# Optimization experiments

Measured on AMD Instinct MI355X. Metric: run time of the kernel, lower is better.

The kernel has to match this reference:

```python
import jax, jax.numpy as jnp
import numpy as np

B, C, N, F_IN = 8, 5, 512, 768
H, D_HID, D_OUT = 4, 128, 64
NEG_SLOPE = 0.2


def _gat_layer(h, mask, W, a_l, a_r, b, apply_relu):
    # h: [B,N,Fin], mask: [B,N,N] bool (mask[b,i,j]=True means edge i->j)
    Bn, Nn, _ = h.shape
    Hh, Dd = a_l.shape
    feat = (h @ W).reshape(Bn, Nn, Hh, Dd)              # [B,N,H,D]
    el = jnp.einsum('bnhd,hd->bnh', feat, a_l)          # src scores
    er = jnp.einsum('bnhd,hd->bnh', feat, a_r)          # dst scores
    e = jax.nn.leaky_relu(el[:, :, None, :] + er[:, None, :, :], NEG_SLOPE)  # [B,src,dst,H]
    m = mask[..., None]
    e = jnp.where(m, e, jnp.finfo(e.dtype).min)
    emax = jnp.max(e, axis=1, keepdims=True)
    p = jnp.where(m, jnp.exp(e - emax), 0.0)
    s = jnp.sum(p, axis=1, keepdims=True)
    alpha = p / jnp.maximum(s, 1e-9)                    # edge softmax over incoming edges per dst
    out = jnp.einsum('bijh,bihd->bjhd', alpha, feat)    # aggregate src features to dst
    out = out + b.reshape(1, 1, Hh, Dd)
    if apply_relu:
        out = jax.nn.relu(out)
    return out                                           # [B,N,H,D]


def setup_inputs() -> dict:
    key = jax.random.key(0)
    ks = jax.random.split(key, 16)
    x = jax.random.normal(ks[0], (B, C, N, F_IN), dtype=jnp.float32)
    adj = (jax.random.uniform(ks[1], (B, C, N, N)) < 0.1).astype(jnp.float32)
    node_nums = jnp.full((B,), N, dtype=jnp.int32)
    s = 0.02
    W0 = jax.random.normal(ks[2], (C, F_IN, H * D_HID)) * s
    al0 = jax.random.normal(ks[3], (C, H, D_HID)) * s
    ar0 = jax.random.normal(ks[4], (C, H, D_HID)) * s
    b0 = jnp.zeros((C, H * D_HID), jnp.float32)
    W1 = jax.random.normal(ks[5], (C, H * D_HID, H * D_HID)) * s
    al1 = jax.random.normal(ks[6], (C, H, D_HID)) * s
    ar1 = jax.random.normal(ks[7], (C, H, D_HID)) * s
    b1 = jnp.zeros((C, H * D_HID), jnp.float32)
    W2 = jax.random.normal(ks[8], (C, H * D_HID, H * D_OUT)) * s
    al2 = jax.random.normal(ks[9], (C, H, D_OUT)) * s
    ar2 = jax.random.normal(ks[10], (C, H, D_OUT)) * s
    b2 = jnp.zeros((C, H * D_OUT), jnp.float32)
    return dict(x=x, adj=adj, W0=W0, al0=al0, ar0=ar0, b0=b0,
                W1=W1, al1=al1, ar1=ar1, b1=b1,
                W2=W2, al2=al2, ar2=ar2, b2=b2, node_nums=node_nums)


def reference(x, adj, W0, al0, ar0, b0, W1, al1, ar1, b1, W2, al2, ar2, b2, node_nums):
    # Original concatenates per-batch node slices and takes channel 0 features only.
    h0 = x[:, 0]                       # [B,N,F_IN]
    logits_all = []
    for c in range(C):
        mask = adj[:, c] > 0           # [B,N,N]
        h = _gat_layer(h0, mask, W0[c], al0[c], ar0[c], b0[c].reshape(H, D_HID), True).reshape(B, N, H * D_HID)
        h = _gat_layer(h, mask, W1[c], al1[c], ar1[c], b1[c].reshape(H, D_HID), True).reshape(B, N, H * D_HID)
        out = _gat_layer(h, mask, W2[c], al2[c], ar2[c], b2[c].reshape(H, D_OUT), False).mean(axis=2)  # [B,N,D_OUT]
        logits_all.append(out)
    return jnp.concatenate(logits_all, axis=-1)  # [B,N,C*D_OUT]
```

## Files before the change

kernel.cpp:

```cpp
#include <hip/hip_runtime.h>

typedef unsigned int uint;
typedef unsigned short ushort_t;
typedef __attribute__((ext_vector_type(8))) short short8;
typedef __attribute__((ext_vector_type(4))) float f32x4;

#define NB 8
#define NC 5
#define NN 512
#define FIN 768
#define NH 4
#define MT 4096
#define LOG2E 1.4426950408889634f

#if __has_builtin(__builtin_amdgcn_exp2f)
#define EXP2F(v) __builtin_amdgcn_exp2f(v)
#else
#define EXP2F(v) __expf((v)*0.6931471805599453f)
#endif

__device__ __forceinline__ float b2f(ushort_t u){ uint x = ((uint)u)<<16; return __builtin_bit_cast(float, x); }
__device__ __forceinline__ ushort_t f2b(float f){
  uint u = __builtin_bit_cast(uint, f);
  u += 0x7FFFu + ((u>>16)&1u);
  return (ushort_t)(u>>16);
}
__device__ __forceinline__ ushort_t f2b_fast(float f){
  uint u = __builtin_bit_cast(uint, f);
  return (ushort_t)((u + 0x8000u)>>16);
}

#define GLL16(gp, lp) __builtin_amdgcn_global_load_lds( \
    (const __attribute__((address_space(1))) void*)(gp), \
    (__attribute__((address_space(3))) void*)(lp), 16, 0, 0)

__global__ __launch_bounds__(256) void prep(const float* __restrict__ x, ushort_t* __restrict__ h0b,
                                            const float* __restrict__ W0, ushort_t* __restrict__ Wt0,
                                            const float* __restrict__ W1, ushort_t* __restrict__ Wt1,
                                            const float* __restrict__ W2, ushort_t* __restrict__ Wt2,
                                            const float* __restrict__ adj, uint* __restrict__ adjB){
  __shared__ float tile[32][33];
  int bid = blockIdx.x, t = threadIdx.x;
  if (bid < 3072){
    int tid = bid*256 + t;
    int row = tid/192, q = tid%192;
    int b = row >> 9, n = row & 511;
    float4 v = *(const float4*)(x + ((size_t)(b*NC)*NN + n)*FIN + q*4);
    ushort4 o; o.x = f2b(v.x); o.y = f2b(v.y); o.z = f2b(v.z); o.w = f2b(v.w);
    *(ushort4*)(h0b + (size_t)row*FIN + q*4) = o;
  } else if (bid < 6912){
    const float* W; ushort_t* Wt; int K, N, c, x0, y0;
    if (bid < 4992){ int l = bid-3072; K=768; N=512; W=W0; Wt=Wt0; c=l/384; int r=l%384; x0=r%16; y0=r/16; }
    else if (bid < 6272){ int l = bid-4992; K=512; N=512; W=W1; Wt=Wt1; c=l/256; int r=l%256; x0=r%16; y0=r/16; }
    else { int l = bid-6272; K=512; N=256; W=W2; Wt=Wt2; c=l/128; int r=l%128; x0=r%8; y0=r/8; }
    int n0 = x0*32, k0 = y0*32;
    int tx = t & 31, ty = t >> 5;
    const float* Wp = W + (size_t)c*K*N;
    ushort_t* Wtp = Wt + (size_t)c*K*N;
    #pragma unroll
    for (int r=0;r<4;r++) tile[ty+r*8][tx] = Wp[(size_t)(k0+ty+r*8)*N + n0+tx];
    __syncthreads();
    #pragma unroll
    for (int r=0;r<4;r++) Wtp[(size_t)(n0+ty+r*8)*K + k0+tx] = f2b(tile[tx][ty+r*8]);
  } else {
    int l = bid - 6912;
    int iw = l & 15, zz = l >> 4;
    const float* ap = adj + (size_t)zz*NN*NN + (size_t)iw*32*NN;
    uint w0 = 0, w1 = 0;
    #pragma unroll 8
    for (int q=0;q<32;q++){
      if (ap[(size_t)q*NN + t]       > 0.f) w0 |= (1u<<q);
      if (ap[(size_t)q*NN + t + 256] > 0.f) w1 |= (1u<<q);
    }
    adjB[((size_t)zz*16 + iw)*512 + t]       = w0;
    adjB[((size_t)zz*16 + iw)*512 + t + 256] = w1;
  }
}

__global__ __launch_bounds__(256) void gemm_tn(const ushort_t* __restrict__ A,
                                               const ushort_t* __restrict__ Bt,
                                               ushort_t* __restrict__ Ob,
                                               int K, long a_cs, long b_cs, int DT){
  __shared__ __align__(16) char smem[128*136*2];
  ushort_t* As = (ushort_t*)smem;
  ushort_t* Bs = As + 128*32;
  ushort_t* St = (ushort_t*)smem;
  int c = blockIdx.z;
  const ushort_t* Ap = A + (size_t)c*a_cs;
  const ushort_t* Bp = Bt + (size_t)c*b_cs;
  int m0 = blockIdx.y*128, n0 = blockIdx.x*128;
  int t = threadIdx.x, lane = t & 63, w = t >> 6;
  int l15 = lane & 15, quad = lane >> 4;
  int wm = (w & 1)*64, wn = (w >> 1)*64;
  f32x4 acc[4][4] = {};
  for (int k0 = 0; k0 < K; k0 += 32){
    __syncthreads();
    {
      int i = t;
      GLL16(Ap + (size_t)(m0 + (i>>2))*K + k0 + (i&3)*8, As + (size_t)(w*64)*8);
      GLL16(Bp + (size_t)(n0 + (i>>2))*K + k0 + (i&3)*8, Bs + (size_t)(w*64)*8);
      i = t + 256;
      GLL16(Ap + (size_t)(m0 + (i>>2))*K + k0 + (i&3)*8, As + (size_t)(w*64 + 256)*8);
      GLL16(Bp + (size_t)(n0 + (i>>2))*K + k0 + (i&3)*8, Bs + (size_t)(w*64 + 256)*8);
    }
    __syncthreads();
    short8 af[4], bfr[4];
    #pragma unroll
    for (int im=0; im<4; im++) af[im] = *(const short8*)(As + (size_t)(wm + im*16 + l15)*32 + quad*8);
    #pragma unroll
    for (int in=0; in<4; in++) bfr[in] = *(const short8*)(Bs + (size_t)(wn + in*16 + l15)*32 + quad*8);
    #pragma unroll
    for (int im=0; im<4; im++)
      #pragma unroll
      for (int in=0; in<4; in++)
        acc[im][in] = __builtin_amdgcn_mfma_f32_16x16x32_bf16(af[im], bfr[in], acc[im][in], 0, 0, 0);
  }
  __syncthreads();
  #pragma unroll
  for (int im=0; im<4; im++)
    #pragma unroll
    for (int in=0; in<4; in++){
      int n = wn + in*16 + l15;
      #pragma unroll
      for (int r=0; r<4; r++){
        int m = wm + im*16 + quad*4 + r;
        St[(size_t)n*136 + m] = f2b(acc[im][in][r]);
      }
    }
  __syncthreads();
  int n_loc = t >> 1, half = t & 1;
  const ushort_t* srcp = St + (size_t)n_loc*136 + half*64;
  ushort_t* dstc = Ob + (size_t)c*MT*DT;
  #pragma unroll
  for (int q=0;q<8;q++){
    size_t g = (size_t)(m0>>3) + half*8 + q;
    *(short8*)(dstc + (g*DT + n0 + n_loc)*8) = *(const short8*)(srcp + q*8);
  }
}

template<int DH>
__global__ __launch_bounds__(256) void eler(const ushort_t* __restrict__ featB,
                                            const float* __restrict__ al, const float* __restrict__ ar,
                                            float* __restrict__ elc, float* __restrict__ erc){
  constexpr int DT = NH*DH;
  __shared__ float als[DH], ars[DH];
  int by = blockIdx.y; int c = by>>2, h = by&3;
  int t = threadIdx.x;
  int m = blockIdx.x*256 + t;
  if (t < DH){ als[t] = al[(size_t)(c*NH+h)*DH + t]; ars[t] = ar[(size_t)(c*NH+h)*DH + t]; }
  __syncthreads();
  const ushort_t* fp = featB + (((size_t)(c*512 + (m>>3))*DT + h*DH))*8 + (m&7);
  float sl = 0.f, sr = 0.f;
  #pragma unroll 8
  for (int d=0; d<DH; d++){
    float f = b2f(fp[(size_t)d*8]);
    sl += f*als[d]; sr += f*ars[d];
  }
  size_t idx = (size_t)(c*NH+h)*MT + m;
  elc[idx] = sl*LOG2E; erc[idx] = sr*LOG2E;
}

template<int DH, int RELU>
__global__ __launch_bounds__(256,4) void agg(const ushort_t* __restrict__ featB,
                                             const uint* __restrict__ adjB,
                                             const float* __restrict__ elc, const float* __restrict__ erc,
                                             const float* __restrict__ bias,
                                             ushort_t* __restrict__ outp){
  constexpr int DT = NH*DH;
  constexpr int BN = DH/16;
  __shared__ __align__(16) ushort_t Fs[2][8*DH*8];
  __shared__ float el_s[512];
  __shared__ uint  Ms[16*64];
  int bid = blockIdx.x;
  int g = bid % 160, jt = bid / 160;
  int c = g>>5, b = (g>>2)&7, h = g&3;
  int zz = b*NC + c;
  int j0 = jt*64;
  int t = threadIdx.x, lane = t&63, w = t>>6, l15 = lane&15, quad = lane>>4;
  size_t eb = (size_t)(c*NH + h)*MT + b*NN;
  const ushort_t* fBc = featB + ((size_t)(c*512 + b*64)*DT + h*DH)*8;
  el_s[t] = elc[eb + t]; el_s[t+256] = elc[eb + t+256];
  #pragma unroll
  for (int k=0;k<4;k++){
    int idx = k*256 + t;
    Ms[idx] = adjB[((size_t)zz*16 + (idx>>6))*512 + j0 + (idx&63)];
  }
  float erv = erc[eb + j0 + w*16 + l15];
  short8 onesv;
  #pragma unroll
  for (int q=0;q<8;q++) onesv[q] = (short)0x3F80;
  f32x4 acc[BN] = {};
  f32x4 accs = {0.f,0.f,0.f,0.f};
  #pragma unroll
  for (int u=0; u<DH/32; u++){
    int gi = w*(DH/32)+u, isub = gi/(DH/64), part = gi%(DH/64);
    GLL16(fBc + (size_t)isub*DT*8 + part*512 + lane*8, &Fs[0][isub*(DH*8) + part*512]);
  }
  __syncthreads();
  for (int ic = 0; ic < 8; ic++){
    int buf = ic & 1;
    if (ic < 7){
      #pragma unroll
      for (int u=0; u<DH/32; u++){
        int gi = w*(DH/32)+u, isub = gi/(DH/64), part = gi%(DH/64);
        GLL16(fBc + (size_t)((ic+1)*8+isub)*DT*8 + part*512 + lane*8, &Fs[buf^1][isub*(DH*8) + part*512]);
      }
    }
    #pragma unroll
    for (int st=0; st<2; st++){
      int i0c = ic*64 + st*32;
      uint mby = (Ms[(i0c>>5)*64 + (w*16+l15)] >> (quad*8)) & 0xFFu;
      float4 ea = *(const float4*)&el_s[i0c + quad*8];
      float4 eb4 = *(const float4*)&el_s[i0c + quad*8 + 4];
      float ev[8] = {ea.x,ea.y,ea.z,ea.w,eb4.x,eb4.y,eb4.z,eb4.w};
      short8 af;
      #pragma unroll
      for (int q=0;q<8;q++){
        float s = ev[q] + erv;
        float lr = fmaxf(s, 0.2f*s);
        float p = EXP2F(lr);
        p = ((mby>>q)&1u) ? p : 0.f;
        af[q] = (short)f2b_fast(p);
      }
      accs = __builtin_amdgcn_mfma_f32_16x16x32_bf16(af, onesv, accs, 0, 0, 0);
      #pragma unroll
      for (int in=0; in<BN; in++){
        short8 bfr = *(const short8*)&Fs[buf][(st*4+quad)*(DH*8) + (in*16+l15)*8];
        acc[in] = __builtin_amdgcn_mfma_f32_16x16x32_bf16(af, bfr, acc[in], 0, 0, 0);
      }
    }
    __syncthreads();
  }
  ushort_t* op = outp + ((size_t)c*MT + b*NN + j0 + w*16)*DT + h*DH;
  float bv[BN];
  #pragma unroll
  for (int in=0; in<BN; in++) bv[in] = bias[(size_t)c*DT + h*DH + in*16 + l15];
  #pragma unroll
  for (int r=0; r<4; r++){
    int jr = quad*4 + r;
    float sinv = 1.f / fmaxf(accs[r], 1e-9f);
    #pragma unroll
    for (int in=0; in<BN; in++){
      float o = acc[in][r]*sinv + bv[in];
      if (RELU) o = fmaxf(o, 0.f);
      op[(size_t)jr*DT + in*16 + l15] = f2b_fast(o);
    }
  }
}

__global__ __launch_bounds__(256) void meank(const ushort_t* __restrict__ h2, float* __restrict__ outp){
  int tid = blockIdx.x*256 + threadIdx.x;
  if (tid >= MT*NC*64) return;
  int d = tid & 63; int r = tid >> 6; int c = r % NC; int m = r / NC;
  const ushort_t* p = h2 + ((size_t)c*MT + m)*256 + d;
  float s = 0.25f*(b2f(p[0]) + b2f(p[64]) + b2f(p[128]) + b2f(p[192]));
  outp[(size_t)m*(NC*64) + c*64 + d] = s;
}

extern "C" void kernel_launch(void* const* d_in, const int* in_sizes, int n_in,
                              void* d_out, int out_size, void* d_ws, size_t ws_size,
                              hipStream_t stream){
  const float* x   = (const float*)d_in[0];
  const float* adj = (const float*)d_in[1];
  const float* W0  = (const float*)d_in[2];
  const float* al0 = (const float*)d_in[3];
  const float* ar0 = (const float*)d_in[4];
  const float* b0  = (const float*)d_in[5];
  const float* W1  = (const float*)d_in[6];
  const float* al1 = (const float*)d_in[7];
  const float* ar1 = (const float*)d_in[8];
  const float* b1  = (const float*)d_in[9];
  const float* W2  = (const float*)d_in[10];
  const float* al2 = (const float*)d_in[11];
  const float* ar2 = (const float*)d_in[12];
  const float* b2  = (const float*)d_in[13];

  ushort_t* h0b  = (ushort_t*)d_ws;
  ushort_t* Wt0  = h0b  + (size_t)MT*FIN;
  ushort_t* Wt1  = Wt0  + (size_t)5*512*768;
  ushort_t* Wt2  = Wt1  + (size_t)5*512*512;
  ushort_t* featB= Wt2  + (size_t)5*256*512;
  ushort_t* hnat = featB+ (size_t)5*(size_t)MT*512;
  uint*     adjB = (uint*)(hnat + (size_t)5*(size_t)MT*512);
  float*    elc  = (float*)(adjB + (size_t)40*16*512);
  float*    erc  = elc + (size_t)NC*NH*MT;

  prep<<<7552, 256, 0, stream>>>(x, h0b, W0, Wt0, W1, Wt1, W2, Wt2, adj, adjB);

  gemm_tn<<<dim3(4,32,5), 256, 0, stream>>>(h0b, Wt0, featB, 768, 0L, (long)512*768, 512);
  eler<128><<<dim3(16,20), 256, 0, stream>>>(featB, al0, ar0, elc, erc);
  agg<128,1><<<1280, 256, 0, stream>>>(featB, adjB, elc, erc, b0, hnat);
  gemm_tn<<<dim3(4,32,5), 256, 0, stream>>>(hnat, Wt1, featB, 512, (long)MT*512, (long)512*512, 512);
  eler<128><<<dim3(16,20), 256, 0, stream>>>(featB, al1, ar1, elc, erc);
  agg<128,1><<<1280, 256, 0, stream>>>(featB, adjB, elc, erc, b1, hnat);
  gemm_tn<<<dim3(2,32,5), 256, 0, stream>>>(hnat, Wt2, featB, 512, (long)MT*512, (long)256*512, 256);
  eler<64><<<dim3(16,20), 256, 0, stream>>>(featB, al2, ar2, elc, erc);
  agg<64,0><<<1280, 256, 0, stream>>>(featB, adjB, elc, erc, b2, hnat);

  meank<<<5120, 256, 0, stream>>>(hnat, (float*)d_out);
}
```

Measured before the change: 314.4 us.

## Fuse attention score computation into GEMM epilogue and factor exp into precomputed products

Removes the separate eler kernels by computing el/er dot products in the GEMM epilogue from the staged bf16 tile, and also precomputes exp(el), exp(0.2 el), exp(er), exp(0.2 er). The aggregation kernel then forms leaky-relu exponentials as products instead of per-edge exp, and loads adjacency mask words directly into registers instead of LDS. This cuts kernel launches and the featB reread and shortens agg's inner loop. In exchange it adds epilogue work and extra global buffers, and the exp products could overflow without max subtraction.

New measurement: 303.7 us. -3.4%, faster.

```diff
diff --git a/kernel.cpp b/kernel.cpp
--- a/kernel.cpp
+++ b/kernel.cpp
@@ -11,13 +11,6 @@
 #define FIN 768
 #define NH 4
 #define MT 4096
-#define LOG2E 1.4426950408889634f
-
-#if __has_builtin(__builtin_amdgcn_exp2f)
-#define EXP2F(v) __builtin_amdgcn_exp2f(v)
-#else
-#define EXP2F(v) __expf((v)*0.6931471805599453f)
-#endif
 
 __device__ __forceinline__ float b2f(ushort_t u){ uint x = ((uint)u)<<16; return __builtin_bit_cast(float, x); }
 __device__ __forceinline__ ushort_t f2b(float f){
@@ -77,11 +70,17 @@
   }
 }
 
+template<int DH>
 __global__ __launch_bounds__(256) void gemm_tn(const ushort_t* __restrict__ A,
                                                const ushort_t* __restrict__ Bt,
                                                ushort_t* __restrict__ Ob,
-                                               int K, long a_cs, long b_cs, int DT){
+                                               const float* __restrict__ al, const float* __restrict__ ar,
+                                               float* __restrict__ el, float* __restrict__ E1, float* __restrict__ E2,
+                                               float* __restrict__ er, float* __restrict__ R1, float* __restrict__ R2,
+                                               int K, long a_cs, long b_cs){
+  constexpr int DT = NH*DH;
   __shared__ __align__(16) char smem[128*136*2];
+  __shared__ float als_s[128], ars_s[128];
   ushort_t* As = (ushort_t*)smem;
   ushort_t* Bs = As + 128*32;
   ushort_t* St = (ushort_t*)smem;
@@ -92,6 +91,10 @@
   int t = threadIdx.x, lane = t & 63, w = t >> 6;
   int l15 = lane & 15, quad = lane >> 4;
   int wm = (w & 1)*64, wn = (w >> 1)*64;
+  if (t < 128){
+    als_s[t] = al[(size_t)c*NH*DH + n0 + t];
+    ars_s[t] = ar[(size_t)c*NH*DH + n0 + t];
+  }
   f32x4 acc[4][4] = {};
   for (int k0 = 0; k0 < K; k0 += 32){
     __syncthreads();
@@ -128,49 +131,53 @@
       }
     }
   __syncthreads();
-  int n_loc = t >> 1, half = t & 1;
-  const ushort_t* srcp = St + (size_t)n_loc*136 + half*64;
-  ushort_t* dstc = Ob + (size_t)c*MT*DT;
-  #pragma unroll
-  for (int q=0;q<8;q++){
-    size_t g = (size_t)(m0>>3) + half*8 + q;
-    *(short8*)(dstc + (g*DT + n0 + n_loc)*8) = *(const short8*)(srcp + q*8);
-  }
-}
-
-template<int DH>
-__global__ __launch_bounds__(256) void eler(const ushort_t* __restrict__ featB,
-                                            const float* __restrict__ al, const float* __restrict__ ar,
-                                            float* __restrict__ elc, float* __restrict__ erc){
-  constexpr int DT = NH*DH;
-  __shared__ float als[DH], ars[DH];
-  int by = blockIdx.y; int c = by>>2, h = by&3;
-  int t = threadIdx.x;
-  int m = blockIdx.x*256 + t;
-  if (t < DH){ als[t] = al[(size_t)(c*NH+h)*DH + t]; ars[t] = ar[(size_t)(c*NH+h)*DH + t]; }
-  __syncthreads();
-  const ushort_t* fp = featB + (((size_t)(c*512 + (m>>3))*DT + h*DH))*8 + (m&7);
-  float sl = 0.f, sr = 0.f;
-  #pragma unroll 8
-  for (int d=0; d<DH; d++){
-    float f = b2f(fp[(size_t)d*8]);
-    sl += f*als[d]; sr += f*ars[d];
-  }
-  size_t idx = (size_t)(c*NH+h)*MT + m;
-  elc[idx] = sl*LOG2E; erc[idx] = sr*LOG2E;
+  {
+    int n_loc = t >> 1, half = t & 1;
+    const ushort_t* srcp = St + (size_t)n_loc*136 + half*64;
+    ushort_t* dstc = Ob + (size_t)c*MT*DT;
+    #pragma unroll
+    for (int q=0;q<8;q++){
+      size_t g = (size_t)(m0>>3) + half*8 + q;
+      *(short8*)(dstc + (g*DT + n0 + n_loc)*8) = *(const short8*)(srcp + q*8);
+    }
+  }
+  {
+    int m = t >> 1, half = t & 1;
+    float sl = 0.f, sr = 0.f;
+    const ushort_t* stp = St + (size_t)(half*64)*136 + m;
+    #pragma unroll 8
+    for (int nn=0; nn<64; nn++){
+      float f = b2f(stp[(size_t)nn*136]);
+      int n = half*64 + nn;
+      sl += f*als_s[n]; sr += f*ars_s[n];
+    }
+    size_t base = (size_t)c*NH*MT;
+    if (DH == 128){
+      sl += __shfl_xor(sl, 1); sr += __shfl_xor(sr, 1);
+      size_t idx = base + (size_t)(n0>>7)*MT + m0 + m;
+      if (half == 0){ el[idx]=sl; E1[idx]=__expf(sl); E2[idx]=__expf(0.2f*sl); }
+      else          { er[idx]=sr; R1[idx]=__expf(sr); R2[idx]=__expf(0.2f*sr); }
+    } else {
+      size_t idx = base + (size_t)((n0>>6)+half)*MT + m0 + m;
+      el[idx]=sl; E1[idx]=__expf(sl); E2[idx]=__expf(0.2f*sl);
+      er[idx]=sr; R1[idx]=__expf(sr); R2[idx]=__expf(0.2f*sr);
+    }
+  }
 }
 
 template<int DH, int RELU>
 __global__ __launch_bounds__(256,4) void agg(const ushort_t* __restrict__ featB,
                                              const uint* __restrict__ adjB,
-                                             const float* __restrict__ elc, const float* __restrict__ erc,
+                                             const float* __restrict__ el, const float* __restrict__ E1,
+                                             const float* __restrict__ E2,
+                                             const float* __restrict__ er, const float* __restrict__ R1,
+                                             const float* __restrict__ R2,
                                              const float* __restrict__ bias,
                                              ushort_t* __restrict__ outp){
   constexpr int DT = NH*DH;
   constexpr int BN = DH/16;
   __shared__ __align__(16) ushort_t Fs[2][8*DH*8];
-  __shared__ float el_s[512];
-  __shared__ uint  Ms[16*64];
+  __shared__ float el_s[512], E1_s[512], E2_s[512];
   int bid = blockIdx.x;
   int g = bid % 160, jt = bid / 160;
   int c = g>>5, b = (g>>2)&7, h = g&3;
@@ -179,13 +186,16 @@
   int t = threadIdx.x, lane = t&63, w = t>>6, l15 = lane&15, quad = lane>>4;
   size_t eb = (size_t)(c*NH + h)*MT + b*NN;
   const ushort_t* fBc = featB + ((size_t)(c*512 + b*64)*DT + h*DH)*8;
-  el_s[t] = elc[eb + t]; el_s[t+256] = elc[eb + t+256];
-  #pragma unroll
-  for (int k=0;k<4;k++){
-    int idx = k*256 + t;
-    Ms[idx] = adjB[((size_t)zz*16 + (idx>>6))*512 + j0 + (idx&63)];
-  }
-  float erv = erc[eb + j0 + w*16 + l15];
+  el_s[t] = el[eb + t]; el_s[t+256] = el[eb + t+256];
+  E1_s[t] = E1[eb + t]; E1_s[t+256] = E1[eb + t+256];
+  E2_s[t] = E2[eb + t]; E2_s[t+256] = E2[eb + t+256];
+  int jme = j0 + w*16 + l15;
+  float erv = er[eb + jme];
+  float R1v = R1[eb + jme];
+  float R2v = R2[eb + jme];
+  uint mw[16];
+  #pragma unroll
+  for (int iw=0; iw<16; iw++) mw[iw] = adjB[((size_t)zz*16 + iw)*512 + jme];
   short8 onesv;
   #pragma unroll
   for (int q=0;q<8;q++) onesv[q] = (short)0x3F80;
@@ -209,16 +219,21 @@
     #pragma unroll
     for (int st=0; st<2; st++){
       int i0c = ic*64 + st*32;
-      uint mby = (Ms[(i0c>>5)*64 + (w*16+l15)] >> (quad*8)) & 0xFFu;
-      float4 ea = *(const float4*)&el_s[i0c + quad*8];
+      uint mby = (mw[i0c>>5] >> (quad*8)) & 0xFFu;
+      float4 ea  = *(const float4*)&el_s[i0c + quad*8];
       float4 eb4 = *(const float4*)&el_s[i0c + quad*8 + 4];
-      float ev[8] = {ea.x,ea.y,ea.z,ea.w,eb4.x,eb4.y,eb4.z,eb4.w};
+      float4 x1a = *(const float4*)&E1_s[i0c + quad*8];
+      float4 x1b = *(const float4*)&E1_s[i0c + quad*8 + 4];
+      float4 x2a = *(const float4*)&E2_s[i0c + quad*8];
+      float4 x2b = *(const float4*)&E2_s[i0c + quad*8 + 4];
+      float ev[8]  = {ea.x,ea.y,ea.z,ea.w,eb4.x,eb4.y,eb4.z,eb4.w};
+      float e1v[8] = {x1a.x,x1a.y,x1a.z,x1a.w,x1b.x,x1b.y,x1b.z,x1b.w};
+      float e2v[8] = {x2a.x,x2a.y,x2a.z,x2a.w,x2b.x,x2b.y,x2b.z,x2b.w};
       short8 af;
       #pragma unroll
       for (int q=0;q<8;q++){
         float s = ev[q] + erv;
-        float lr = fmaxf(s, 0.2f*s);
-        float p = EXP2F(lr);
+        float p = (s > 0.f) ? (e1v[q]*R1v) : (e2v[q]*R2v);
         p = ((mby>>q)&1u) ? p : 0.f;
         af[q] = (short)f2b_fast(p);
       }
@@ -282,20 +297,27 @@
   ushort_t* featB= Wt2  + (size_t)5*256*512;
   ushort_t* hnat = featB+ (size_t)5*(size_t)MT*512;
   uint*     adjB = (uint*)(hnat + (size_t)5*(size_t)MT*512);
-  float*    elc  = (float*)(adjB + (size_t)40*16*512);
-  float*    erc  = elc + (size_t)NC*NH*MT;
+  float*    elp  = (float*)(adjB + (size_t)40*16*512);
+  float*    E1p  = elp + (size_t)NC*NH*MT;
+  float*    E2p  = E1p + (size_t)NC*NH*MT;
+  float*    erp  = E2p + (size_t)NC*NH*MT;
+  float*    R1p  = erp + (size_t)NC*NH*MT;
+  float*    R2p  = R1p + (size_t)NC*NH*MT;
 
   prep<<<7552, 256, 0, stream>>>(x, h0b, W0, Wt0, W1, Wt1, W2, Wt2, adj, adjB);
 
-  gemm_tn<<<dim3(4,32,5), 256, 0, stream>>>(h0b, Wt0, featB, 768, 0L, (long)512*768, 512);
-  eler<128><<<dim3(16,20), 256, 0, stream>>>(featB, al0, ar0, elc, erc);
-  agg<128,1><<<1280, 256, 0, stream>>>(featB, adjB, elc, erc, b0, hnat);
-  gemm_tn<<<dim3(4,32,5), 256, 0, stream>>>(hnat, Wt1, featB, 512, (long)MT*512, (long)512*512, 512);
-  eler<128><<<dim3(16,20), 256, 0, stream>>>(featB, al1, ar1, elc, erc);
-  agg<128,1><<<1280, 256, 0, stream>>>(featB, adjB, elc, erc, b1, hnat);
-  gemm_tn<<<dim3(2,32,5), 256, 0, stream>>>(hnat, Wt2, featB, 512, (long)MT*512, (long)256*512, 256);
-  eler<64><<<dim3(16,20), 256, 0, stream>>>(featB, al2, ar2, elc, erc);
-  agg<64,0><<<1280, 256, 0, stream>>>(featB, adjB, elc, erc, b2, hnat);
+  gemm_tn<128><<<dim3(4,32,5), 256, 0, stream>>>(h0b, Wt0, featB, al0, ar0,
+                                                 elp, E1p, E2p, erp, R1p, R2p,
+                                                 768, 0L, (long)512*768);
+  agg<128,1><<<1280, 256, 0, stream>>>(featB, adjB, elp, E1p, E2p, erp, R1p, R2p, b0, hnat);
+  gemm_tn<128><<<dim3(4,32,5), 256, 0, stream>>>(hnat, Wt1, featB, al1, ar1,
+                                                 elp, E1p, E2p, erp, R1p, R2p,
+                                                 512, (long)MT*512, (long)512*512);
+  agg<128,1><<<1280, 256, 0, stream>>>(featB, adjB, elp, E1p, E2p, erp, R1p, R2p, b1, hnat);
+  gemm_tn<64><<<dim3(2,32,5), 256, 0, stream>>>(hnat, Wt2, featB, al2, ar2,
+                                                elp, E1p, E2p, erp, R1p, R2p,
+                                                512, (long)MT*512, (long)256*512);
+  agg<64,0><<<1280, 256, 0, stream>>>(featB, adjB, elp, E1p, E2p, erp, R1p, R2p, b2, hnat);
 
   meank<<<5120, 256, 0, stream>>>(hnat, (float*)d_out);
 }
```
